# Kernel optimization log

Hardware: AMD Instinct MI355X
Metric: run time of the kernel (lower is better)

Reference implementation:

```python
import jax, jax.numpy as jnp
import numpy as np

B, T, V, E, H, N = 8, 128, 32000, 128, 256, 20
SHARPEN = 5.0
EPS = 1e-8  # torch cosine_similarity eps


def setup_inputs() -> dict:
    key = jax.random.key(0)
    ks = jax.random.split(key, 8)
    g = lambda k, shape, scale: (jax.random.normal(k, shape, dtype=jnp.float32) * scale)
    return {
        "x_ids": jax.random.randint(ks[0], (B, T), 0, V),
        "emb": g(ks[1], (V, E), 0.02),                 # nn.Embedding weight
        "W_i": g(ks[2], (H, E), E ** -0.5),            # rnn_i weight (no bias)
        "W_h": g(ks[3], (H, H), H ** -0.5),            # rnn_h weight
        "W_fc": g(ks[4], (V, 2 * H), (2 * H) ** -0.5), # fc -> vocab (softmaxed)
        "W_ops": g(ks[5], (3, 2 * H), (2 * H) ** -0.5),
        "W_choose": g(ks[6], (2, 2 * H), (2 * H) ** -0.5),
        "sharp": jnp.array([SHARPEN], dtype=jnp.float32),
    }


def _l2norm(x, eps=1e-12):
    # F.normalize(x, dim=-1)
    n = jnp.linalg.norm(x, axis=-1, keepdims=True)
    return x / jnp.maximum(n, eps)


def reference(x_ids, emb, W_i, W_h, W_fc, W_ops, W_choose, sharp):
    x = emb[x_ids]                                   # [B,T,E]
    # pre-normalize vocab rows for cosine-sim readout (clamped like torch)
    emb_cn = emb / jnp.maximum(jnp.linalg.norm(emb, axis=1, keepdims=True), EPS)
    sh = sharp[0]

    stack0 = jnp.full((B, N, E), 0.001, dtype=x.dtype)      # zero_offset + 0.001
    ptr0 = jnp.zeros((B, N), x.dtype).at[:, 0].set(1.0)     # pointer at slot 0
    h0 = jnp.zeros((B, H), x.dtype)

    def step(carry, xi):
        h, stack, ptr = carry
        ri = _l2norm(xi) @ W_i.T                     # rnn_i(normalize(x_t))
        h = jnp.tanh(ri + h @ W_h.T)
        hm = 1.0 - jax.nn.relu(h)
        hmod = jnp.concatenate([hm, hm], axis=1)     # [B,2H]
        # GumbelSoftmax(temp=1, hard=False) -> deterministic softmax (no noise)
        ops = jax.nn.softmax(hmod @ W_ops.T, axis=1)  # [B,3]
        push, pop, nop = ops[:, 0], ops[:, 1], ops[:, 2]
        # --- differentiable stack push/pop/nop ---
        pop_val = jnp.einsum('bn,bne->be', ptr, stack)      # soft read at pointer
        p_push = jnp.roll(ptr, 1, axis=1)
        p_pop = jnp.roll(ptr, -1, axis=1)
        new_ptr = push[:, None] * p_push + pop[:, None] * p_pop + nop[:, None] * ptr
        new_ptr = jnp.clip(new_ptr, EPS) ** sh              # sharpen
        new_ptr = new_ptr / jnp.sum(new_ptr, axis=1, keepdims=True)
        w = (push[:, None] * p_push)[:, :, None]            # write weight [B,N,1]
        new_stack = stack * (1.0 - w) + w * xi[:, None, :]
        # --- readout ---
        semantic = jax.nn.softmax(hmod @ W_fc.T, axis=1)    # [B,V]
        pv_n = pop_val / jnp.maximum(
            jnp.linalg.norm(pop_val, axis=1, keepdims=True), EPS)
        syntactic = pv_n @ emb_cn.T                          # cosine sim [B,V]
        choice = jax.nn.softmax(hmod @ W_choose.T, axis=1)   # [B,2]
        out = choice[:, 0:1] * semantic + choice[:, 1:2] * syntactic
        return (h, new_stack, new_ptr), out

    _, outs = jax.lax.scan(step, (h0, stack0, ptr0), jnp.swapaxes(x, 0, 1))
    return jnp.swapaxes(outs, 0, 1)  # [B,T,V]
```

## Files before the change

kernel.cpp:

```cpp
#include <hip/hip_runtime.h>
#include <hip/hip_bf16.h>
#include <stdint.h>

#define T_ 128
#define B_ 8
#define V_ 32000
#define E_ 128
#define H_ 256
#define N_ 20
#define M_ 1024
#define PIT 264
#define PIT2 136
#define NCH5 500

typedef __attribute__((ext_vector_type(8))) short short8;
typedef __attribute__((ext_vector_type(4))) float f32x4;
typedef unsigned short ushort;

static __device__ __forceinline__ ushort f2bf_u(float f) {
  __hip_bfloat16 h = __float2bfloat16(f);
  return *reinterpret_cast<ushort*>(&h);
}

__global__ void prep_k(const float* __restrict__ Wh, uint4* __restrict__ whb4,
                       const float* __restrict__ Wi, float* __restrict__ WiT) {
  if (blockIdx.x < 32) {
    int idx = blockIdx.x*256 + threadIdx.x;
    int k8 = idx >> 8, i = idx & 255;
    const float* s = Wh + i*H_ + k8*8;
    uint4 o;
    o.x = (uint32_t)f2bf_u(s[0]) | ((uint32_t)f2bf_u(s[1]) << 16);
    o.y = (uint32_t)f2bf_u(s[2]) | ((uint32_t)f2bf_u(s[3]) << 16);
    o.z = (uint32_t)f2bf_u(s[4]) | ((uint32_t)f2bf_u(s[5]) << 16);
    o.w = (uint32_t)f2bf_u(s[6]) | ((uint32_t)f2bf_u(s[7]) << 16);
    whb4[idx] = o;
  } else {
    int idx = (blockIdx.x - 32)*256 + threadIdx.x;
    if (idx < H_*E_) {
      int i = idx >> 7, e = idx & (E_-1);
      WiT[e*H_ + i] = Wi[idx];
    }
  }
}

__global__ __launch_bounds__(256) void ri_k(const int* __restrict__ x_ids,
    const float* __restrict__ emb, const float* __restrict__ WiT,
    float* __restrict__ RI)
{
  __shared__ float xn[E_];
  __shared__ float red[2];
  int r = blockIdx.x, tid = threadIdx.x;
  int id = x_ids[r];
  float v = 0.f;
  if (tid < E_) v = emb[id*E_ + tid];
  float ss = v*v;
  if (tid < E_) {
    #pragma unroll
    for (int off = 32; off >= 1; off >>= 1) ss += __shfl_xor(ss, off);
    if ((tid & 63) == 0) red[tid >> 6] = ss;
  }
  __syncthreads();
  float inv = 1.f / fmaxf(sqrtf(red[0] + red[1]), 1e-12f);
  if (tid < E_) xn[tid] = v*inv;
  __syncthreads();
  float s = 0.f;
  for (int e = 0; e < E_; ++e) s += xn[e]*WiT[e*H_ + tid];
  RI[r*H_ + tid] = s;
}

__global__ __launch_bounds__(1024) void chain_k(
    const uint4* __restrict__ whb4, const float* __restrict__ RI,
    float* __restrict__ HMf, ushort* __restrict__ HMb,
    const float* __restrict__ Wfc, const float* __restrict__ emb,
    ushort* __restrict__ Wfcb, ushort* __restrict__ embnb)
{
  __shared__ uint4 wlds[32*256];
  __shared__ __align__(16) float hbuf[2][H_];
  __shared__ float hred[3][H_];
  const int tid = threadIdx.x;

  if (blockIdx.x >= B_) {
    const int nb = gridDim.x - B_;
    const int bx = blockIdx.x - B_;
    for (long idx = (long)bx*1024 + tid; idx < (long)V_*H_; idx += (long)nb*1024) {
      int n = idx >> 8, k = idx & 255;
      Wfcb[idx] = f2bf_u(Wfc[(size_t)n*2*H_ + k] + Wfc[(size_t)n*2*H_ + H_ + k]);
    }
    const int wv = tid >> 6, l = tid & 63;
    for (int v = bx*16 + wv; v < V_; v += nb*16) {
      float e0 = emb[(size_t)v*E_ + l];
      float e1 = emb[(size_t)v*E_ + 64 + l];
      float ss = e0*e0 + e1*e1;
      #pragma unroll
      for (int off = 32; off >= 1; off >>= 1) ss += __shfl_xor(ss, off);
      float inv = 1.f / fmaxf(sqrtf(ss), 1e-8f);
      embnb[(size_t)v*E_ + l]      = f2bf_u(e0*inv);
      embnb[(size_t)v*E_ + 64 + l] = f2bf_u(e1*inv);
    }
    return;
  }

  const int b = blockIdx.x;
  const int q = tid >> 8, i = tid & 255;

  for (int m = tid; m < 32*256; m += 1024) wlds[m] = whb4[m];
  if (q == 0) hbuf[0][i] = 0.f;
  __syncthreads();
  float ri_c = (q == 0) ? RI[(size_t)b*T_*H_ + i] : 0.f;

  for (int t = 0; t < T_; ++t) {
    const int r = b*T_ + t;
    float ri_n = 0.f;
    if (q == 0 && t+1 < T_) ri_n = RI[(size_t)(r+1)*H_ + i];
    const float4* h4 = reinterpret_cast<const float4*>(hbuf[t & 1]);
    float p0 = 0.f, p1 = 0.f, p2 = 0.f, p3 = 0.f;
    #pragma unroll
    for (int j = 0; j < 8; ++j) {
      uint4 w = wlds[(q*8 + j)*256 + i];
      float4 ha = h4[q*16 + 2*j];
      float4 hb = h4[q*16 + 2*j + 1];
      p0 += __uint_as_float(w.x << 16)*ha.x + __uint_as_float(w.x & 0xffff0000u)*ha.y;
      p1 += __uint_as_float(w.y << 16)*ha.z + __uint_as_float(w.y & 0xffff0000u)*ha.w;
      p2 += __uint_as_float(w.z << 16)*hb.x + __uint_as_float(w.z & 0xffff0000u)*hb.y;
      p3 += __uint_as_float(w.w << 16)*hb.z + __uint_as_float(w.w & 0xffff0000u)*hb.w;
    }
    float p = (p0 + p1) + (p2 + p3);
    if (q) hred[q-1][i] = p;
    __syncthreads();
    if (q == 0) {
      float s = ri_c + p + hred[0][i] + hred[1][i] + hred[2][i];
      float hn = tanhf(s);
      hbuf[(t+1) & 1][i] = hn;
      float hm = 1.f - fmaxf(hn, 0.f);
      HMf[(size_t)r*H_ + i] = hm;
      HMb[(size_t)r*H_ + i] = f2bf_u(hm);
    }
    ri_c = ri_n;
    __syncthreads();
  }
}

__global__ __launch_bounds__(256) void stats6_k(const ushort* __restrict__ HMb,
    const ushort* __restrict__ Wfcb, const float* __restrict__ HMf,
    const float* __restrict__ W_ops, const float* __restrict__ W_ch,
    const float* __restrict__ sharp, const int* __restrict__ x_ids,
    const float* __restrict__ emb,
    float* __restrict__ SS, float* __restrict__ CH, float* __restrict__ PV,
    ushort* __restrict__ PVNb)
{
  __shared__ __align__(16) char smem[64*PIT*2];
  const int tid = threadIdx.x;
  const int wave = tid >> 6, lane = tid & 63;
  const int lr = lane & 15, g = lane >> 4;

  if (blockIdx.y == 0) {
    if (blockIdx.x >= B_) return;
    float*  ops_l = (float*)smem;
    float2* pw_l  = (float2*)(smem + 2048);
    int*    ids_l = (int*)(smem + 2048 + 20480);
    const int b = blockIdx.x;
    float wo[5][4];
    #pragma unroll
    for (int k = 0; k < 3; ++k)
      #pragma unroll
      for (int j = 0; j < 4; ++j)
        wo[k][j] = W_ops[k*2*H_ + 4*lane + j] + W_ops[k*2*H_ + H_ + 4*lane + j];
    #pragma unroll
    for (int k = 0; k < 2; ++k)
      #pragma unroll
      for (int j = 0; j < 4; ++j)
        wo[3+k][j] = W_ch[k*2*H_ + 4*lane + j] + W_ch[k*2*H_ + H_ + 4*lane + j];
    if (tid < T_) ids_l[tid] = x_ids[b*T_ + tid];
    for (int rl = wave*32; rl < wave*32 + 32; ++rl) {
      int R = b*T_ + rl;
      float4 hm4 = reinterpret_cast<const float4*>(HMf + (size_t)R*H_)[lane];
      float d0 = hm4.x*wo[0][0] + hm4.y*wo[0][1] + hm4.z*wo[0][2] + hm4.w*wo[0][3];
      float d1 = hm4.x*wo[1][0] + hm4.y*wo[1][1] + hm4.z*wo[1][2] + hm4.w*wo[1][3];
      float d2 = hm4.x*wo[2][0] + hm4.y*wo[2][1] + hm4.z*wo[2][2] + hm4.w*wo[2][3];
      float d3 = hm4.x*wo[3][0] + hm4.y*wo[3][1] + hm4.z*wo[3][2] + hm4.w*wo[3][3];
      float d4 = hm4.x*wo[4][0] + hm4.y*wo[4][1] + hm4.z*wo[4][2] + hm4.w*wo[4][3];
      #pragma unroll
      for (int off = 32; off >= 1; off >>= 1) {
        d0 += __shfl_xor(d0, off); d1 += __shfl_xor(d1, off); d2 += __shfl_xor(d2, off);
        d3 += __shfl_xor(d3, off); d4 += __shfl_xor(d4, off);
      }
      if (lane == 0) {
        float mx = fmaxf(d0, fmaxf(d1, d2));
        float e0 = expf(d0-mx), e1 = expf(d1-mx), e2 = expf(d2-mx);
        float oi = 1.f/(e0+e1+e2);
        ops_l[rl*4+0] = e0*oi; ops_l[rl*4+1] = e1*oi; ops_l[rl*4+2] = e2*oi;
        float cm = fmaxf(d3, d4);
        float f0 = expf(d3-cm), f1 = expf(d4-cm);
        float ci = 1.f/(f0+f1);
        CH[R*2] = f0*ci; CH[R*2+1] = f1*ci;
      }
    }
    __syncthreads();
    if (tid < 64) {
      const float sh = sharp[0];
      float ptr = (tid == 0) ? 1.f : 0.f;
      const int lp = (tid + N_ - 1) % N_, ln = (tid + 1) % N_;
      for (int t = 0; t < T_; ++t) {
        float push = ops_l[t*4+0], pop = ops_l[t*4+1], nop = ops_l[t*4+2];
        float pp = __shfl(ptr, lp);
        float po = __shfl(ptr, ln);
        float wgt = push*pp;
        float raw = wgt + pop*po + nop*ptr;
        float np = 0.f;
        if (tid < N_) np = exp2f(sh * log2f(fmaxf(raw, 1e-8f)));
        float ssum = np;
        #pragma unroll
        for (int off = 1; off < 32; off <<= 1) ssum += __shfl_xor(ssum, off);
        if (tid < N_) {
          pw_l[t*N_ + tid] = make_float2(ptr, wgt);
          ptr = np / ssum;
        }
      }
    }
    __syncthreads();
    if (tid < E_) {
      const int e = tid;
      float stck[N_];
      #pragma unroll
      for (int n = 0; n < N_; ++n) stck[n] = 0.001f;
      float xi_c = emb[(size_t)ids_l[0]*E_ + e];
      for (int t = 0; t < T_; ++t) {
        float xi_n = (t+1 < T_) ? emb[(size_t)ids_l[t+1]*E_ + e] : 0.f;
        float pv = 0.f;
        #pragma unroll
        for (int n = 0; n < N_; ++n) {
          float2 pw = pw_l[t*N_ + n];
          pv += pw.x * stck[n];
          stck[n] += pw.y * (xi_c - stck[n]);
        }
        PV[(size_t)(b*T_ + t)*E_ + e] = pv;
        xi_c = xi_n;
      }
    }
    __threadfence_block();
    __syncthreads();
    for (int rl = wave*32; rl < wave*32 + 32; ++rl) {
      int R = b*T_ + rl;
      float a = PV[(size_t)R*E_ + lane];
      float c = PV[(size_t)R*E_ + 64 + lane];
      float ss = a*a + c*c;
      #pragma unroll
      for (int off = 32; off >= 1; off >>= 1) ss += __shfl_xor(ss, off);
      float inv = 1.f / fmaxf(sqrtf(ss), 1e-8f);
      PVNb[(size_t)R*E_ + lane]      = f2bf_u(a*inv);
      PVNb[(size_t)R*E_ + 64 + lane] = f2bf_u(c*inv);
    }
    return;
  }

  ushort* Bs = (ushort*)smem;
  const int Cb = blockIdx.x*64;
  {
    const uint4* srcB = (const uint4*)(Wfcb + (size_t)Cb*H_);
    #pragma unroll
    for (int it = 0; it < 8; ++it) {
      int idx = it*256 + tid, row = idx >> 5, c = idx & 31;
      *(uint4*)&Bs[row*PIT + c*8] = srcB[row*32 + c];
    }
  }
  const int Rw = (blockIdx.y - 1)*256 + wave*64;
  __syncthreads();
  f32x4 acc[4][4] = {};
  #pragma unroll
  for (int ks = 0; ks < 8; ++ks) {
    short8 a0 = *(const short8*)(HMb + (size_t)(Rw + 0*16 + lr)*H_ + ks*32 + g*8);
    short8 a1 = *(const short8*)(HMb + (size_t)(Rw + 1*16 + lr)*H_ + ks*32 + g*8);
    short8 a2 = *(const short8*)(HMb + (size_t)(Rw + 2*16 + lr)*H_ + ks*32 + g*8);
    short8 a3 = *(const short8*)(HMb + (size_t)(Rw + 3*16 + lr)*H_ + ks*32 + g*8);
    short8 b0 = *(const short8*)(&Bs[(0*16 + lr)*PIT + ks*32 + g*8]);
    short8 b1 = *(const short8*)(&Bs[(1*16 + lr)*PIT + ks*32 + g*8]);
    short8 b2 = *(const short8*)(&Bs[(2*16 + lr)*PIT + ks*32 + g*8]);
    short8 b3 = *(const short8*)(&Bs[(3*16 + lr)*PIT + ks*32 + g*8]);
    #define MF(mi, av) \
      acc[mi][0] = __builtin_amdgcn_mfma_f32_16x16x32_bf16(av, b0, acc[mi][0], 0, 0, 0); \
      acc[mi][1] = __builtin_amdgcn_mfma_f32_16x16x32_bf16(av, b1, acc[mi][1], 0, 0, 0); \
      acc[mi][2] = __builtin_amdgcn_mfma_f32_16x16x32_bf16(av, b2, acc[mi][2], 0, 0, 0); \
      acc[mi][3] = __builtin_amdgcn_mfma_f32_16x16x32_bf16(av, b3, acc[mi][3], 0, 0, 0);
    MF(0, a0) MF(1, a1) MF(2, a2) MF(3, a3)
    #undef MF
  }
  #pragma unroll
  for (int mi = 0; mi < 4; ++mi)
    #pragma unroll
    for (int r = 0; r < 4; ++r) {
      float s = expf(acc[mi][0][r]) + expf(acc[mi][1][r])
              + expf(acc[mi][2][r]) + expf(acc[mi][3][r]);
      #pragma unroll
      for (int off = 1; off < 16; off <<= 1) s += __shfl_xor(s, off);
      if (lr == 0) SS[(size_t)blockIdx.x*M_ + (Rw + mi*16 + g*4 + r)] = s;
    }
}

__global__ void reduce5_k(const float* __restrict__ SS, float* __restrict__ MS) {
  int row = blockIdx.x, l = threadIdx.x;
  float s = 0.f;
  for (int c = l; c < NCH5; c += 64) s += SS[(size_t)c*M_ + row];
  #pragma unroll
  for (int off = 32; off >= 1; off >>= 1) s += __shfl_xor(s, off);
  if (l == 0) MS[row] = 1.f/s;
}

__global__ __launch_bounds__(256) void final6_k(const ushort* __restrict__ HMb,
    const ushort* __restrict__ Wfcb, const ushort* __restrict__ PVNb,
    const ushort* __restrict__ embnb, const float* __restrict__ MS,
    const float* __restrict__ CH, float* __restrict__ out)
{
  __shared__ __align__(16) ushort Bs[64*PIT];
  const int tid = threadIdx.x;
  const int Cb = blockIdx.x*64;
  const int wave = tid >> 6, lane = tid & 63;
  const int lr = lane & 15, g = lane >> 4;
  const int Rw = blockIdx.y*256 + wave*64;

  {
    const uint4* srcB = (const uint4*)(Wfcb + (size_t)Cb*H_);
    #pragma unroll
    for (int it = 0; it < 8; ++it) {
      int idx = it*256 + tid, row = idx >> 5, c = idx & 31;
      *(uint4*)&Bs[row*PIT + c*8] = srcB[row*32 + c];
    }
  }
  __syncthreads();
  f32x4 accL[4][4] = {};
  #pragma unroll
  for (int ks = 0; ks < 8; ++ks) {
    short8 a0 = *(const short8*)(HMb + (size_t)(Rw + 0*16 + lr)*H_ + ks*32 + g*8);
    short8 a1 = *(const short8*)(HMb + (size_t)(Rw + 1*16 + lr)*H_ + ks*32 + g*8);
    short8 a2 = *(const short8*)(HMb + (size_t)(Rw + 2*16 + lr)*H_ + ks*32 + g*8);
    short8 a3 = *(const short8*)(HMb + (size_t)(Rw + 3*16 + lr)*H_ + ks*32 + g*8);
    short8 b0 = *(const short8*)(&Bs[(0*16 + lr)*PIT + ks*32 + g*8]);
    short8 b1 = *(const short8*)(&Bs[(1*16 + lr)*PIT + ks*32 + g*8]);
    short8 b2 = *(const short8*)(&Bs[(2*16 + lr)*PIT + ks*32 + g*8]);
    short8 b3 = *(const short8*)(&Bs[(3*16 + lr)*PIT + ks*32 + g*8]);
    #define MFL(mi, av) \
      accL[mi][0] = __builtin_amdgcn_mfma_f32_16x16x32_bf16(av, b0, accL[mi][0], 0, 0, 0); \
      accL[mi][1] = __builtin_amdgcn_mfma_f32_16x16x32_bf16(av, b1, accL[mi][1], 0, 0, 0); \
      accL[mi][2] = __builtin_amdgcn_mfma_f32_16x16x32_bf16(av, b2, accL[mi][2], 0, 0, 0); \
      accL[mi][3] = __builtin_amdgcn_mfma_f32_16x16x32_bf16(av, b3, accL[mi][3], 0, 0, 0);
    MFL(0, a0) MFL(1, a1) MFL(2, a2) MFL(3, a3)
    #undef MFL
  }
  __syncthreads();

  {
    const uint4* srcB = (const uint4*)(embnb + (size_t)Cb*E_);
    #pragma unroll
    for (int it = 0; it < 4; ++it) {
      int idx = it*256 + tid, row = idx >> 4, c = idx & 15;
      *(uint4*)&Bs[row*PIT2 + c*8] = srcB[row*16 + c];
    }
  }
  __syncthreads();
  f32x4 accS[4][4] = {};
  #pragma unroll
  for (int ks = 0; ks < 4; ++ks) {
    short8 a0 = *(const short8*)(PVNb + (size_t)(Rw + 0*16 + lr)*E_ + ks*32 + g*8);
    short8 a1 = *(const short8*)(PVNb + (size_t)(Rw + 1*16 + lr)*E_ + ks*32 + g*8);
    short8 a2 = *(const short8*)(PVNb + (size_t)(Rw + 2*16 + lr)*E_ + ks*32 + g*8);
    short8 a3 = *(const short8*)(PVNb + (size_t)(Rw + 3*16 + lr)*E_ + ks*32 + g*8);
    short8 b0 = *(const short8*)(&Bs[(0*16 + lr)*PIT2 + ks*32 + g*8]);
    short8 b1 = *(const short8*)(&Bs[(1*16 + lr)*PIT2 + ks*32 + g*8]);
    short8 b2 = *(const short8*)(&Bs[(2*16 + lr)*PIT2 + ks*32 + g*8]);
    short8 b3 = *(const short8*)(&Bs[(3*16 + lr)*PIT2 + ks*32 + g*8]);
    #define MFS(mi, av) \
      accS[mi][0] = __builtin_amdgcn_mfma_f32_16x16x32_bf16(av, b0, accS[mi][0], 0, 0, 0); \
      accS[mi][1] = __builtin_amdgcn_mfma_f32_16x16x32_bf16(av, b1, accS[mi][1], 0, 0, 0); \
      accS[mi][2] = __builtin_amdgcn_mfma_f32_16x16x32_bf16(av, b2, accS[mi][2], 0, 0, 0); \
      accS[mi][3] = __builtin_amdgcn_mfma_f32_16x16x32_bf16(av, b3, accS[mi][3], 0, 0, 0);
    MFS(0, a0) MFS(1, a1) MFS(2, a2) MFS(3, a3)
    #undef MFS
  }

  #pragma unroll
  for (int mi = 0; mi < 4; ++mi)
    #pragma unroll
    for (int r = 0; r < 4; ++r) {
      int row = Rw + mi*16 + g*4 + r;
      float Si = MS[row];
      float c0 = CH[row*2], c1 = CH[row*2+1];
      size_t base = (size_t)row*V_ + Cb + lr;
      #pragma unroll
      for (int nj = 0; nj < 4; ++nj)
        out[base + nj*16] = c0*expf(accL[mi][nj][r])*Si + c1*accS[mi][nj][r];
    }
}

extern "C" void kernel_launch(void* const* d_in, const int* in_sizes, int n_in,
                              void* d_out, int out_size, void* d_ws, size_t ws_size,
                              hipStream_t stream) {
  const int*   x_ids = (const int*)d_in[0];
  const float* emb   = (const float*)d_in[1];
  const float* W_i   = (const float*)d_in[2];
  const float* W_h   = (const float*)d_in[3];
  const float* W_fc  = (const float*)d_in[4];
  const float* W_ops = (const float*)d_in[5];
  const float* W_ch  = (const float*)d_in[6];
  const float* sharp = (const float*)d_in[7];
  float* out = (float*)d_out;

  float* ws    = (float*)d_ws;
  uint4*  whb4 = (uint4*)ws;
  float*  WiT  = ws + 65536;
  float*  RI   = WiT + 32768;
  float*  CH   = RI + 262144;
  float*  MS   = CH + 2048;
  float*  SS   = MS + 1024;
  float*  HMf  = SS + 512000;
  float*  PV   = HMf + 262144;
  float*  fend = PV + 131072;
  ushort* HMb   = (ushort*)fend;
  ushort* PVNb  = HMb + 262144;
  ushort* Wfcb  = PVNb + 131072;
  ushort* embnb = Wfcb + 8192000;

  prep_k <<<160, 256, 0, stream>>>(W_h, whb4, W_i, WiT);
  ri_k   <<<M_, 256, 0, stream>>>(x_ids, emb, WiT, RI);
  chain_k<<<248, 1024, 0, stream>>>(whb4, RI, HMf, HMb, W_fc, emb, Wfcb, embnb);
  stats6_k<<<dim3(NCH5, 5), 256, 0, stream>>>(HMb, Wfcb, HMf, W_ops, W_ch, sharp,
                                              x_ids, emb, SS, CH, PV, PVNb);
  reduce5_k<<<M_, 64, 0, stream>>>(SS, MS);
  final6_k<<<dim3(NCH5, M_/256), 256, 0, stream>>>(HMb, Wfcb, PVNb, embnb, MS, CH, out);
}
```

Before: 380.5 us.

## Run all batch recurrences in one block with MFMA and split-bf16 hidden state

The sequential RNN recurrence moves from eight 1024-thread blocks, one per batch row and each doing scalar dot products, to a single 512-thread block. That block advances all batch rows together with bf16 MFMA instructions, keeping the W_h fragments in registers. The hidden state is kept as a bf16 high part plus a bf16 residual in the A-operand rows, which recovers close to fp32 accuracy, and the two partial products are summed with a lane shuffle. The other 240 blocks still convert the W_fc and embedding weights. The aim is to shorten the 128-step serial critical path, at the cost of some precision risk from the bf16 weights and split state.

```diff
diff --git a/kernel.cpp b/kernel.cpp
--- a/kernel.cpp
+++ b/kernel.cpp
@@ -68,26 +68,24 @@
   RI[r*H_ + tid] = s;
 }
 
-__global__ __launch_bounds__(1024) void chain_k(
+__global__ __launch_bounds__(512, 1) void chainm_k(
     const uint4* __restrict__ whb4, const float* __restrict__ RI,
     float* __restrict__ HMf, ushort* __restrict__ HMb,
     const float* __restrict__ Wfc, const float* __restrict__ emb,
     ushort* __restrict__ Wfcb, ushort* __restrict__ embnb)
 {
-  __shared__ uint4 wlds[32*256];
-  __shared__ __align__(16) float hbuf[2][H_];
-  __shared__ float hred[3][H_];
+  __shared__ __align__(16) ushort hbuf[2][16][PIT];
   const int tid = threadIdx.x;
 
-  if (blockIdx.x >= B_) {
-    const int nb = gridDim.x - B_;
-    const int bx = blockIdx.x - B_;
-    for (long idx = (long)bx*1024 + tid; idx < (long)V_*H_; idx += (long)nb*1024) {
+  if (blockIdx.x >= 1) {
+    const int nb = gridDim.x - 1;
+    const int bx = blockIdx.x - 1;
+    for (long idx = (long)bx*512 + tid; idx < (long)V_*H_; idx += (long)nb*512) {
       int n = idx >> 8, k = idx & 255;
       Wfcb[idx] = f2bf_u(Wfc[(size_t)n*2*H_ + k] + Wfc[(size_t)n*2*H_ + H_ + k]);
     }
     const int wv = tid >> 6, l = tid & 63;
-    for (int v = bx*16 + wv; v < V_; v += nb*16) {
+    for (int v = bx*8 + wv; v < V_; v += nb*8) {
       float e0 = emb[(size_t)v*E_ + l];
       float e1 = emb[(size_t)v*E_ + 64 + l];
       float ss = e0*e0 + e1*e1;
@@ -100,42 +98,64 @@
     return;
   }
 
-  const int b = blockIdx.x;
-  const int q = tid >> 8, i = tid & 255;
-
-  for (int m = tid; m < 32*256; m += 1024) wlds[m] = whb4[m];
-  if (q == 0) hbuf[0][i] = 0.f;
-  __syncthreads();
-  float ri_c = (q == 0) ? RI[(size_t)b*T_*H_ + i] : 0.f;
+  const int wv = tid >> 6, l = tid & 63;
+  const int c = l & 15, g = l >> 4;
+  const int nt0 = 2*wv, nt1 = 2*wv + 1;
+
+  short8 bf0[8], bf1[8];
+  #pragma unroll
+  for (int kk = 0; kk < 8; ++kk) {
+    bf0[kk] = *(const short8*)&whb4[(size_t)(kk*4 + g)*256 + nt0*16 + c];
+    bf1[kk] = *(const short8*)&whb4[(size_t)(kk*4 + g)*256 + nt1*16 + c];
+  }
+  for (int m = tid; m < 2*16*PIT; m += 512) ((ushort*)hbuf)[m] = 0;
+  __syncthreads();
 
   for (int t = 0; t < T_; ++t) {
-    const int r = b*T_ + t;
-    float ri_n = 0.f;
-    if (q == 0 && t+1 < T_) ri_n = RI[(size_t)(r+1)*H_ + i];
-    const float4* h4 = reinterpret_cast<const float4*>(hbuf[t & 1]);
-    float p0 = 0.f, p1 = 0.f, p2 = 0.f, p3 = 0.f;
-    #pragma unroll
-    for (int j = 0; j < 8; ++j) {
-      uint4 w = wlds[(q*8 + j)*256 + i];
-      float4 ha = h4[q*16 + 2*j];
-      float4 hb = h4[q*16 + 2*j + 1];
-      p0 += __uint_as_float(w.x << 16)*ha.x + __uint_as_float(w.x & 0xffff0000u)*ha.y;
-      p1 += __uint_as_float(w.y << 16)*ha.z + __uint_as_float(w.y & 0xffff0000u)*ha.w;
-      p2 += __uint_as_float(w.z << 16)*hb.x + __uint_as_float(w.z & 0xffff0000u)*hb.y;
-      p3 += __uint_as_float(w.w << 16)*hb.z + __uint_as_float(w.w & 0xffff0000u)*hb.w;
-    }
-    float p = (p0 + p1) + (p2 + p3);
-    if (q) hred[q-1][i] = p;
-    __syncthreads();
-    if (q == 0) {
-      float s = ri_c + p + hred[0][i] + hred[1][i] + hred[2][i];
-      float hn = tanhf(s);
-      hbuf[(t+1) & 1][i] = hn;
-      float hm = 1.f - fmaxf(hn, 0.f);
-      HMf[(size_t)r*H_ + i] = hm;
-      HMb[(size_t)r*H_ + i] = f2bf_u(hm);
-    }
-    ri_c = ri_n;
+    const int cur = t & 1, nxt = cur ^ 1;
+    float ri[2][4];
+    #pragma unroll
+    for (int tau = 0; tau < 2; ++tau) {
+      int n = (nt0 + tau)*16 + c;
+      #pragma unroll
+      for (int r = 0; r < 4; ++r) {
+        int b = (g & 1)*4 + r;
+        ri[tau][r] = RI[((size_t)b*T_ + t)*H_ + n];
+      }
+    }
+    short8 af[8];
+    #pragma unroll
+    for (int kk = 0; kk < 8; ++kk)
+      af[kk] = *(const short8*)&hbuf[cur][c][kk*32 + g*8];
+    f32x4 acc0 = {}, acc1 = {};
+    #pragma unroll
+    for (int kk = 0; kk < 8; ++kk) {
+      acc0 = __builtin_amdgcn_mfma_f32_16x16x32_bf16(af[kk], bf0[kk], acc0, 0, 0, 0);
+      acc1 = __builtin_amdgcn_mfma_f32_16x16x32_bf16(af[kk], bf1[kk], acc1, 0, 0, 0);
+    }
+    #pragma unroll
+    for (int tau = 0; tau < 2; ++tau) {
+      int n = (nt0 + tau)*16 + c;
+      #pragma unroll
+      for (int r = 0; r < 4; ++r) {
+        float d = tau ? acc1[r] : acc0[r];
+        float s = d + __shfl_xor(d, 32);
+        int b = (g & 1)*4 + r;
+        float hn = tanhf(ri[tau][r] + s);
+        ushort hb16 = f2bf_u(hn);
+        float hif = __uint_as_float((uint32_t)hb16 << 16);
+        int row; ushort val;
+        if (g < 2) {
+          float hm = 1.f - fmaxf(hn, 0.f);
+          HMf[((size_t)b*T_ + t)*H_ + n] = hm;
+          HMb[((size_t)b*T_ + t)*H_ + n] = f2bf_u(hm);
+          row = b; val = hb16;
+        } else {
+          row = b + 8; val = f2bf_u(hn - hif);
+        }
+        hbuf[nxt][row][n] = val;
+      }
+    }
     __syncthreads();
   }
 }
@@ -242,13 +262,13 @@
     for (int rl = wave*32; rl < wave*32 + 32; ++rl) {
       int R = b*T_ + rl;
       float a = PV[(size_t)R*E_ + lane];
-      float c = PV[(size_t)R*E_ + 64 + lane];
-      float ss = a*a + c*c;
+      float cc = PV[(size_t)R*E_ + 64 + lane];
+      float ss = a*a + cc*cc;
       #pragma unroll
       for (int off = 32; off >= 1; off >>= 1) ss += __shfl_xor(ss, off);
       float inv = 1.f / fmaxf(sqrtf(ss), 1e-8f);
       PVNb[(size_t)R*E_ + lane]      = f2bf_u(a*inv);
-      PVNb[(size_t)R*E_ + 64 + lane] = f2bf_u(c*inv);
+      PVNb[(size_t)R*E_ + 64 + lane] = f2bf_u(cc*inv);
     }
     return;
   }
@@ -259,8 +279,8 @@
     const uint4* srcB = (const uint4*)(Wfcb + (size_t)Cb*H_);
     #pragma unroll
     for (int it = 0; it < 8; ++it) {
-      int idx = it*256 + tid, row = idx >> 5, c = idx & 31;
-      *(uint4*)&Bs[row*PIT + c*8] = srcB[row*32 + c];
+      int idx = it*256 + tid, row = idx >> 5, cc = idx & 31;
+      *(uint4*)&Bs[row*PIT + cc*8] = srcB[row*32 + cc];
     }
   }
   const int Rw = (blockIdx.y - 1)*256 + wave*64;
@@ -321,8 +341,8 @@
     const uint4* srcB = (const uint4*)(Wfcb + (size_t)Cb*H_);
     #pragma unroll
     for (int it = 0; it < 8; ++it) {
-      int idx = it*256 + tid, row = idx >> 5, c = idx & 31;
-      *(uint4*)&Bs[row*PIT + c*8] = srcB[row*32 + c];
+      int idx = it*256 + tid, row = idx >> 5, cc = idx & 31;
+      *(uint4*)&Bs[row*PIT + cc*8] = srcB[row*32 + cc];
     }
   }
   __syncthreads();
@@ -351,8 +371,8 @@
     const uint4* srcB = (const uint4*)(embnb + (size_t)Cb*E_);
     #pragma unroll
     for (int it = 0; it < 4; ++it) {
-      int idx = it*256 + tid, row = idx >> 4, c = idx & 15;
-      *(uint4*)&Bs[row*PIT2 + c*8] = srcB[row*16 + c];
+      int idx = it*256 + tid, row = idx >> 4, cc = idx & 15;
+      *(uint4*)&Bs[row*PIT2 + cc*8] = srcB[row*16 + cc];
     }
   }
   __syncthreads();
@@ -420,7 +440,7 @@
 
   prep_k <<<160, 256, 0, stream>>>(W_h, whb4, W_i, WiT);
   ri_k   <<<M_, 256, 0, stream>>>(x_ids, emb, WiT, RI);
-  chain_k<<<248, 1024, 0, stream>>>(whb4, RI, HMf, HMb, W_fc, emb, Wfcb, embnb);
+  chainm_k<<<241, 512, 0, stream>>>(whb4, RI, HMf, HMb, W_fc, emb, Wfcb, embnb);
   stats6_k<<<dim3(NCH5, 5), 256, 0, stream>>>(HMb, Wfcb, HMf, W_ops, W_ch, sharp,
                                               x_ids, emb, SS, CH, PV, PVNb);
   reduce5_k<<<M_, 64, 0, stream>>>(SS, MS);
```

After: 475.1 us. 1.25x slower.
